# Optimization experiments

Measured on AMD Instinct MI355X. Metric: run time of the kernel, lower is better.

## Reference

```python
import jax, jax.numpy as jnp
import numpy as np


def _diff_x(x, r):
    # x: [..., Hp, W]; sliding-window difference of column-cumsum along axis -2
    left = x[..., r:2 * r + 1, :]
    middle = x[..., 2 * r + 1:, :] - x[..., :-2 * r - 1, :]
    right = x[..., -1:, :] - x[..., -2 * r - 1:-r - 1, :]
    return jnp.concatenate([left, middle, right], axis=-2)


def _diff_y(x, r):
    # x: [..., H, Wp]; sliding-window difference along axis -1
    left = x[..., r:2 * r + 1]
    middle = x[..., 2 * r + 1:] - x[..., :-2 * r - 1]
    right = x[..., -1:] - x[..., -2 * r - 1:-r - 1]
    return jnp.concatenate([left, middle, right], axis=-1)


def setup_inputs() -> dict:
    key = jax.random.key(0)
    B, C, H, W = 8, 3, 2048, 2048
    x = jax.random.normal(key, (B, C, H, W), dtype=jnp.float32)
    return {"x": x, "r": 4}


def reference(x, r):
    # reflect pad r on both spatial dims (PyTorch 'reflect' == numpy 'reflect')
    xp = jnp.pad(x, ((0, 0), (0, 0), (r, r), (r, r)), mode="reflect")
    xp = jnp.cumsum(xp, axis=-2)
    xp = _diff_x(xp, r)
    xp = jnp.cumsum(xp, axis=-1)
    xp = _diff_y(xp, r)
    norm = jnp.asarray((2 * r + 1) ** 2, dtype=x.dtype)
    return xp[..., r:-r, r:-r] / norm
```

## Files before the change

kernel.cpp:

```cpp
#include <hip/hip_runtime.h>


constexpr int H   = 2048;
constexpr int W   = 2048;
constexpr int R   = 4;
constexpr int RH  = 64;
constexpr int TPB = 256;
constexpr int CPT = 4;
constexpr int BCOLS = TPB * CPT;

typedef float f32x4 __attribute__((ext_vector_type(4)));

__device__ __forceinline__ int reflect_row(int r) {
  r = (r < 0) ? -r : r;
  return (r >= H) ? (2 * H - 2 - r) : r;
}

template <int P, bool STORE>
__device__ __forceinline__ void bf_step(
    int s, int r0, int off, int c0, bool doStore,
    const float* __restrict__ px, float* __restrict__ po,
    float (&hbuf)[9][CPT], float (&vsum)[CPT]) {
  const int lr = reflect_row(r0 - R + s);
  const float* __restrict__ rowp = px + (size_t)lr * W;

  const float4 A = *(const float4*)(rowp + off);
  const float4 B = *(const float4*)(rowp + off + 4);
  const float4 C = *(const float4*)(rowp + off + 8);

  float h0 = ((A.x + A.y) + (A.z + A.w)) +
             ((B.x + B.y) + (B.z + B.w)) + C.x;
  float h1 = h0 + C.y - A.x;
  float h2 = h1 + C.z - A.y;
  float h3 = h2 + C.w - A.z;

  vsum[0] += h0 - hbuf[P][0]; hbuf[P][0] = h0;
  vsum[1] += h1 - hbuf[P][1]; hbuf[P][1] = h1;
  vsum[2] += h2 - hbuf[P][2]; hbuf[P][2] = h2;
  vsum[3] += h3 - hbuf[P][3]; hbuf[P][3] = h3;

  if (STORE) {
    if (doStore) {
      const float inv81 = 1.0f / 81.0f;
      float* o = po + (size_t)(r0 + s - 2 * R) * W + c0;
      f32x4 ov = {vsum[0] * inv81, vsum[1] * inv81,
                  vsum[2] * inv81, vsum[3] * inv81};
      __builtin_nontemporal_store(ov, (f32x4*)o);
    }
  }
}

__global__ __launch_bounds__(TPB, 5) void BoxFilter_kernel(
    const float* __restrict__ x, float* __restrict__ out, int nMain) {
  const int t   = threadIdx.x;
  const int bid = blockIdx.x;

  if (bid >= nMain) {
    const int idx   = (bid - nMain) * TPB + t;
    const int plane = idx >> 11;
    const int r     = idx & (H - 1);
    const float* __restrict__ px = x   + (size_t)plane * H * W;
    float*       __restrict__ po = out + (size_t)plane * H * W;

    float accL[4] = {0.f, 0.f, 0.f, 0.f};
    float accR[4] = {0.f, 0.f, 0.f, 0.f};
#pragma unroll
    for (int dr = -R; dr <= R; ++dr) {
      const int rr = reflect_row(r + dr);
      const float* __restrict__ rowp = px + (size_t)rr * W;
      float l[9], m[9];
#pragma unroll
      for (int i = 0; i < 9; ++i) l[i] = rowp[i];
#pragma unroll
      for (int i = 0; i < 9; ++i) m[i] = rowp[W - 9 + i];
#pragma unroll
      for (int c = 0; c < 4; ++c) {
#pragma unroll
        for (int k = -R; k <= R; ++k) {
          int j = c + k; j = (j < 0) ? -j : j;
          accL[c] += l[j];
          int rc = (W - 4 + c) + k;
          rc = (rc >= W) ? (2 * W - 2 - rc) : rc;
          accR[c] += m[rc - (W - 9)];
        }
      }
    }
    const float inv81 = 1.0f / 81.0f;
    float* oL = po + (size_t)r * W;
    float* oR = po + (size_t)r * W + (W - 4);
    f32x4 vL = {accL[0] * inv81, accL[1] * inv81,
                accL[2] * inv81, accL[3] * inv81};
    f32x4 vR = {accR[0] * inv81, accR[1] * inv81,
                accR[2] * inv81, accR[3] * inv81};
    *(f32x4*)oL = vL;
    *(f32x4*)oR = vR;
    return;
  }

  const int lid   = (bid & 7) * (nMain >> 3) + (bid >> 3);
  const int plane = lid >> 6;
  const int rem   = lid & 63;
  const int half  = rem >> 5;
  const int chunk = rem & 31;
  const int r0    = chunk * RH;
  const int cb    = half * BCOLS;
  const float* __restrict__ px = x   + (size_t)plane * H * W;
  float*       __restrict__ po = out + (size_t)plane * H * W;

  const int c0 = cb + t * CPT;
  int off = c0 - R;
  off = off < 0 ? 0 : off;
  off = off > W - 12 ? W - 12 : off;
  const bool doStore = (c0 != 0) && (c0 != W - CPT);

  float hbuf[9][CPT];
  float vsum[CPT];
#pragma unroll
  for (int j = 0; j < CPT; ++j) vsum[j] = 0.0f;
#pragma unroll
  for (int p = 0; p < 9; ++p)
#pragma unroll
    for (int j = 0; j < CPT; ++j) hbuf[p][j] = 0.0f;

  bf_step<0, false>(0, r0, off, c0, doStore, px, po, hbuf, vsum);
  bf_step<1, false>(1, r0, off, c0, doStore, px, po, hbuf, vsum);
  bf_step<2, false>(2, r0, off, c0, doStore, px, po, hbuf, vsum);
  bf_step<3, false>(3, r0, off, c0, doStore, px, po, hbuf, vsum);
  bf_step<4, false>(4, r0, off, c0, doStore, px, po, hbuf, vsum);
  bf_step<5, false>(5, r0, off, c0, doStore, px, po, hbuf, vsum);
  bf_step<6, false>(6, r0, off, c0, doStore, px, po, hbuf, vsum);
  bf_step<7, false>(7, r0, off, c0, doStore, px, po, hbuf, vsum);
  bf_step<8, true>(8, r0, off, c0, doStore, px, po, hbuf, vsum);

#pragma unroll 1
  for (int s0 = 9; s0 <= 63; s0 += 9) {
    bf_step<0, true>(s0 + 0, r0, off, c0, doStore, px, po, hbuf, vsum);
    bf_step<1, true>(s0 + 1, r0, off, c0, doStore, px, po, hbuf, vsum);
    bf_step<2, true>(s0 + 2, r0, off, c0, doStore, px, po, hbuf, vsum);
    bf_step<3, true>(s0 + 3, r0, off, c0, doStore, px, po, hbuf, vsum);
    bf_step<4, true>(s0 + 4, r0, off, c0, doStore, px, po, hbuf, vsum);
    bf_step<5, true>(s0 + 5, r0, off, c0, doStore, px, po, hbuf, vsum);
    bf_step<6, true>(s0 + 6, r0, off, c0, doStore, px, po, hbuf, vsum);
    bf_step<7, true>(s0 + 7, r0, off, c0, doStore, px, po, hbuf, vsum);
    bf_step<8, true>(s0 + 8, r0, off, c0, doStore, px, po, hbuf, vsum);
  }
}

extern "C" void kernel_launch(void* const* d_in, const int* in_sizes, int n_in,
                              void* d_out, int out_size, void* d_ws, size_t ws_size,
                              hipStream_t stream) {
  const float* x   = (const float*)d_in[0];
  float*       out = (float*)d_out;
  const int planes = out_size / (H * W);
  const int nMain  = planes * (H / RH) * 2;
  const int nEdge  = planes * H / TPB;
  dim3 grid(nMain + nEdge);
  dim3 block(TPB);
  hipLaunchKernelGGL(BoxFilter_kernel, grid, block, 0, stream, x, out, nMain);
}
```

Baseline: 179.4 us.

## Software-pipeline row loads three steps ahead and shrink row chunks

Row loads are split out of the compute step into a three-slot register ring, so each step prefetches the row three steps ahead and memory latency overlaps with the sliding-sum arithmetic. Row chunk height is halved from 64 to 32, which raises the share of halo rows re-read per block. The block-to-tile mapping drops the interleaved swizzle so vertically adjacent chunks run as consecutive blocks, which may let L2 serve the halo reads. Launch bounds drop from 5 to 4 waves per SIMD to make room for the extra registers, at some cost in occupancy.

```diff
diff --git a/kernel.cpp b/kernel.cpp
--- a/kernel.cpp
+++ b/kernel.cpp
@@ -4,29 +4,42 @@
 constexpr int H   = 2048;
 constexpr int W   = 2048;
 constexpr int R   = 4;
-constexpr int RH  = 64;
+constexpr int RH  = 32;
 constexpr int TPB = 256;
 constexpr int CPT = 4;
 constexpr int BCOLS = TPB * CPT;
+constexpr int STEPS = RH + 2 * R;
 
 typedef float f32x4 __attribute__((ext_vector_type(4)));
+
+struct Slot { float4 A, B, C; };
 
 __device__ __forceinline__ int reflect_row(int r) {
   r = (r < 0) ? -r : r;
   return (r >= H) ? (2 * H - 2 - r) : r;
 }
 
-template <int P, bool STORE>
+template <int K>
+__device__ __forceinline__ void issue_load(int s, int r0, int off,
+                                           const float* __restrict__ px,
+                                           Slot (&sl)[3]) {
+  const int lr = reflect_row(r0 - R + s);
+  const float* __restrict__ rowp = px + (size_t)lr * W + off;
+  sl[K].A = *(const float4*)(rowp);
+  sl[K].B = *(const float4*)(rowp + 4);
+  sl[K].C = *(const float4*)(rowp + 8);
+}
+
+template <int P, int K, bool STORE, bool PF>
 __device__ __forceinline__ void bf_step(
     int s, int r0, int off, int c0, bool doStore,
     const float* __restrict__ px, float* __restrict__ po,
-    float (&hbuf)[9][CPT], float (&vsum)[CPT]) {
-  const int lr = reflect_row(r0 - R + s);
-  const float* __restrict__ rowp = px + (size_t)lr * W;
+    Slot (&sl)[3], float (&hbuf)[9][CPT], float (&vsum)[CPT]) {
+  const float4 A = sl[K].A;
+  const float4 B = sl[K].B;
+  const float4 C = sl[K].C;
 
-  const float4 A = *(const float4*)(rowp + off);
-  const float4 B = *(const float4*)(rowp + off + 4);
-  const float4 C = *(const float4*)(rowp + off + 8);
+  if (PF) issue_load<K>(s + 3, r0, off, px, sl);
 
   float h0 = ((A.x + A.y) + (A.z + A.w)) +
              ((B.x + B.y) + (B.z + B.w)) + C.x;
@@ -50,7 +63,7 @@
   }
 }
 
-__global__ __launch_bounds__(TPB, 5) void BoxFilter_kernel(
+__global__ __launch_bounds__(TPB, 4) void BoxFilter_kernel(
     const float* __restrict__ x, float* __restrict__ out, int nMain) {
   const int t   = threadIdx.x;
   const int bid = blockIdx.x;
@@ -97,11 +110,10 @@
     return;
   }
 
-  const int lid   = (bid & 7) * (nMain >> 3) + (bid >> 3);
-  const int plane = lid >> 6;
-  const int rem   = lid & 63;
-  const int half  = rem >> 5;
-  const int chunk = rem & 31;
+  const int plane = bid >> 7;
+  const int rem   = bid & 127;
+  const int chunk = rem >> 1;
+  const int half  = rem & 1;
   const int r0    = chunk * RH;
   const int cb    = half * BCOLS;
   const float* __restrict__ px = x   + (size_t)plane * H * W;
@@ -122,28 +134,37 @@
 #pragma unroll
     for (int j = 0; j < CPT; ++j) hbuf[p][j] = 0.0f;
 
-  bf_step<0, false>(0, r0, off, c0, doStore, px, po, hbuf, vsum);
-  bf_step<1, false>(1, r0, off, c0, doStore, px, po, hbuf, vsum);
-  bf_step<2, false>(2, r0, off, c0, doStore, px, po, hbuf, vsum);
-  bf_step<3, false>(3, r0, off, c0, doStore, px, po, hbuf, vsum);
-  bf_step<4, false>(4, r0, off, c0, doStore, px, po, hbuf, vsum);
-  bf_step<5, false>(5, r0, off, c0, doStore, px, po, hbuf, vsum);
-  bf_step<6, false>(6, r0, off, c0, doStore, px, po, hbuf, vsum);
-  bf_step<7, false>(7, r0, off, c0, doStore, px, po, hbuf, vsum);
-  bf_step<8, true>(8, r0, off, c0, doStore, px, po, hbuf, vsum);
+  Slot sl[3];
+  issue_load<0>(0, r0, off, px, sl);
+  issue_load<1>(1, r0, off, px, sl);
+  issue_load<2>(2, r0, off, px, sl);
+
+  bf_step<0, 0, false, true>(0, r0, off, c0, doStore, px, po, sl, hbuf, vsum);
+  bf_step<1, 1, false, true>(1, r0, off, c0, doStore, px, po, sl, hbuf, vsum);
+  bf_step<2, 2, false, true>(2, r0, off, c0, doStore, px, po, sl, hbuf, vsum);
+  bf_step<3, 0, false, true>(3, r0, off, c0, doStore, px, po, sl, hbuf, vsum);
+  bf_step<4, 1, false, true>(4, r0, off, c0, doStore, px, po, sl, hbuf, vsum);
+  bf_step<5, 2, false, true>(5, r0, off, c0, doStore, px, po, sl, hbuf, vsum);
+  bf_step<6, 0, false, true>(6, r0, off, c0, doStore, px, po, sl, hbuf, vsum);
+  bf_step<7, 1, false, true>(7, r0, off, c0, doStore, px, po, sl, hbuf, vsum);
+  bf_step<8, 2, true, true>(8, r0, off, c0, doStore, px, po, sl, hbuf, vsum);
 
 #pragma unroll 1
-  for (int s0 = 9; s0 <= 63; s0 += 9) {
-    bf_step<0, true>(s0 + 0, r0, off, c0, doStore, px, po, hbuf, vsum);
-    bf_step<1, true>(s0 + 1, r0, off, c0, doStore, px, po, hbuf, vsum);
-    bf_step<2, true>(s0 + 2, r0, off, c0, doStore, px, po, hbuf, vsum);
-    bf_step<3, true>(s0 + 3, r0, off, c0, doStore, px, po, hbuf, vsum);
-    bf_step<4, true>(s0 + 4, r0, off, c0, doStore, px, po, hbuf, vsum);
-    bf_step<5, true>(s0 + 5, r0, off, c0, doStore, px, po, hbuf, vsum);
-    bf_step<6, true>(s0 + 6, r0, off, c0, doStore, px, po, hbuf, vsum);
-    bf_step<7, true>(s0 + 7, r0, off, c0, doStore, px, po, hbuf, vsum);
-    bf_step<8, true>(s0 + 8, r0, off, c0, doStore, px, po, hbuf, vsum);
+  for (int s0 = 9; s0 <= 27; s0 += 9) {
+    bf_step<0, 0, true, true>(s0 + 0, r0, off, c0, doStore, px, po, sl, hbuf, vsum);
+    bf_step<1, 1, true, true>(s0 + 1, r0, off, c0, doStore, px, po, sl, hbuf, vsum);
+    bf_step<2, 2, true, true>(s0 + 2, r0, off, c0, doStore, px, po, sl, hbuf, vsum);
+    bf_step<3, 0, true, true>(s0 + 3, r0, off, c0, doStore, px, po, sl, hbuf, vsum);
+    bf_step<4, 1, true, true>(s0 + 4, r0, off, c0, doStore, px, po, sl, hbuf, vsum);
+    bf_step<5, 2, true, true>(s0 + 5, r0, off, c0, doStore, px, po, sl, hbuf, vsum);
+    bf_step<6, 0, true, true>(s0 + 6, r0, off, c0, doStore, px, po, sl, hbuf, vsum);
+    bf_step<7, 1, true, true>(s0 + 7, r0, off, c0, doStore, px, po, sl, hbuf, vsum);
+    bf_step<8, 2, true, true>(s0 + 8, r0, off, c0, doStore, px, po, sl, hbuf, vsum);
   }
+  bf_step<0, 0, true, true >(36, r0, off, c0, doStore, px, po, sl, hbuf, vsum);
+  bf_step<1, 1, true, false>(37, r0, off, c0, doStore, px, po, sl, hbuf, vsum);
+  bf_step<2, 2, true, false>(38, r0, off, c0, doStore, px, po, sl, hbuf, vsum);
+  bf_step<3, 0, true, false>(39, r0, off, c0, doStore, px, po, sl, hbuf, vsum);
 }
 
 extern "C" void kernel_launch(void* const* d_in, const int* in_sizes, int n_in,
```

Result: faster. 171.5 us (-4.5%).
